# Performance work log

Hardware: AMD Instinct MI355X
Metric: run time of the kernel (lower is better)

The kernel has to match this reference:

```python
import jax, jax.numpy as jnp
import numpy as np

LN_EPS = 1e-5

def _layer_norm(x, g, b):
    mu = jnp.mean(x, axis=-1, keepdims=True)
    var = jnp.mean(jnp.square(x - mu), axis=-1, keepdims=True)
    return (x - mu) * jax.lax.rsqrt(var + LN_EPS) * g + b

def setup_inputs() -> dict:
    key = jax.random.key(0)
    ks = jax.random.split(key, 12)
    B, L, E, H, W = 4, 1024, 1024, 16, 128
    s = 0.02
    return {
        "x": jax.random.normal(ks[0], (B, L, E), dtype=jnp.float32),
        "in_proj_w": jax.random.normal(ks[1], (3 * E, E), dtype=jnp.float32) * s,
        "in_proj_b": jnp.zeros((3 * E,), dtype=jnp.float32),
        "out_proj_w": jax.random.normal(ks[2], (E, E), dtype=jnp.float32) * s,
        "out_proj_b": jnp.zeros((E,), dtype=jnp.float32),
        "ln1_g": jnp.ones((E,), dtype=jnp.float32),
        "ln1_b": jnp.zeros((E,), dtype=jnp.float32),
        "w1": jax.random.normal(ks[3], (4 * E, E), dtype=jnp.float32) * s,
        "b1": jnp.zeros((4 * E,), dtype=jnp.float32),
        "w2": jax.random.normal(ks[4], (E, 4 * E), dtype=jnp.float32) * s,
        "b2": jnp.zeros((E,), dtype=jnp.float32),
        "ln2_g": jnp.ones((E,), dtype=jnp.float32),
        "ln2_b": jnp.zeros((E,), dtype=jnp.float32),
        "n_head": 16,
        "window_size": 128,
    }

def reference(x, in_proj_w, in_proj_b, out_proj_w, out_proj_b,
              ln1_g, ln1_b, w1, b1, w2, b2, ln2_g, ln2_b,
              n_head, window_size):
    B, L, E = x.shape
    H = n_head
    D = E // H
    # qkv projection (torch Linear convention: y = x @ W.T + b)
    qkv = jnp.einsum('ble,fe->blf', x, in_proj_w) + in_proj_b  # [B,L,3E]
    q, k, v = jnp.split(qkv, 3, axis=-1)
    q = q.reshape(B, L, H, D).transpose(0, 2, 1, 3)  # [B,H,L,D]
    k = k.reshape(B, L, H, D).transpose(0, 2, 1, 3)
    v = v.reshape(B, L, H, D).transpose(0, 2, 1, 3)
    scores = jnp.einsum('bhld,bhmd->bhlm', q, k) / np.sqrt(D)  # [B,H,L,L]
    # banded window mask: allowed iff |i-j| <= window_size (same as the double loop)
    idx = jnp.arange(L)
    band = jnp.abs(idx[:, None] - idx[None, :]) <= window_size  # [L,L]
    scores = jnp.where(band[None, None], scores, -jnp.inf)
    attn = jax.nn.softmax(scores, axis=-1)  # [B,H,L,L]
    ctx = jnp.einsum('bhlm,bhmd->bhld', attn, v)  # [B,H,L,D]
    ctx = ctx.transpose(0, 2, 1, 3).reshape(B, L, E)
    attn_out = jnp.einsum('ble,fe->blf', ctx, out_proj_w) + out_proj_b
    attn_weights = jnp.mean(attn, axis=1)  # torch MHA averages heads -> [B,L,L]
    # residual + norm1 (dropout is identity in eval)
    h = _layer_norm(x + attn_out, ln1_g, ln1_b)
    # positionwise FFN
    ff = jnp.einsum('ble,fe->blf', h, w1) + b1
    ff = jax.nn.relu(ff)
    ff = jnp.einsum('blf,ef->ble', ff, w2) + b2
    out = _layer_norm(h + ff, ln2_g, ln2_b)
    return (out, attn_weights)
```

## Files before the change

kernel.cpp:

```cpp
#include <hip/hip_runtime.h>

#define BB 4
#define LL 1024
#define EE 1024
#define HH 16
#define DD 64

typedef __attribute__((ext_vector_type(8))) short short8;
typedef __attribute__((ext_vector_type(4))) float floatx4;

#define PSTR ((size_t)4096 * 1024)

__device__ __forceinline__ float bf2f(short s) {
    union { unsigned u; float f; } c;
    c.u = ((unsigned)(unsigned short)s) << 16;
    return c.f;
}
__device__ __forceinline__ short f2bf(float f) {
    union { float f; unsigned u; } c; c.f = f;
    unsigned r = c.u + 0x7fffu + ((c.u >> 16) & 1u);
    return (short)(r >> 16);
}

__device__ __forceinline__ void async_copy16(const void* g, void* l) {
    __builtin_amdgcn_global_load_lds(
        (const __attribute__((address_space(1))) unsigned int*)g,
        (__attribute__((address_space(3))) unsigned int*)l, 16, 0, 0);
}

__global__ __launch_bounds__(256) void cvt5(
    const float* __restrict__ x, const float* __restrict__ wqkv,
    const float* __restrict__ wo, const float* __restrict__ w1,
    const float* __restrict__ w2,
    short* __restrict__ xb, short* __restrict__ wqkvb, short* __restrict__ wob,
    short* __restrict__ w1b, short* __restrict__ w2b)
{
    int bi = blockIdx.x;
    const float* in; short* out; int base;
    if      (bi <  4096) { in = x;    out = xb;    base = 0;     }
    else if (bi <  7168) { in = wqkv; out = wqkvb; base = 4096;  }
    else if (bi <  8192) { in = wo;   out = wob;   base = 7168;  }
    else if (bi < 12288) { in = w1;   out = w1b;   base = 8192;  }
    else                 { in = w2;   out = w2b;   base = 12288; }
    int i = (bi - base) * 256 + threadIdx.x;
    float4 v = ((const float4*)in)[i];
    unsigned long long u =
          (unsigned long long)(unsigned short)f2bf(v.x)
        | ((unsigned long long)(unsigned short)f2bf(v.y) << 16)
        | ((unsigned long long)(unsigned short)f2bf(v.z) << 32)
        | ((unsigned long long)(unsigned short)f2bf(v.w) << 48);
    ((unsigned long long*)out)[i] = u;
}

template<bool RELU, bool SK>
__global__ __launch_bounds__(512, 2) void gemm256(
    const short* __restrict__ A, const short* __restrict__ Bw,
    const float* __restrict__ bias,
    short* __restrict__ Cb,
    int M, int N, int K, int Ksp)
{
    __shared__ short SH[67584];
    const int tid  = threadIdx.x;
    const int w    = tid >> 6, lane = tid & 63;
    const int fr   = lane & 15, quad = lane >> 4;
    const int wm   = w >> 2,  wn   = w & 3;

    const int gx   = gridDim.x;
    const int flat = blockIdx.y * gx + blockIdx.x;
    const int nwg  = gx * gridDim.y;
    const int q8   = nwg >> 3;
    const int swz  = (flat & 7) * q8 + (flat >> 3);
    const int m0   = (swz % gx) * 256;
    const int n0   = (swz / gx) * 256;

    const int kb = SK ? blockIdx.z * Ksp : 0;
    const int NT = (SK ? Ksp : K) >> 6;

    const int srow = w * 16 + (lane >> 3);
    const int gcol = ((lane & 7) ^ ((lane >> 3) & 7)) * 8;

    auto stage = [&](int s, int h) {
        if (s >= NT) return;
        short* dstb = SH + (s & 1) * 32768 + (h >> 1) * 16384 + (h & 1) * 8192 + w * 1024;
        const short* src = (h < 2)
            ? A  + (size_t)(m0 + h * 128 + srow) * K + kb + s * 64 + gcol
            : Bw + (size_t)(n0 + (h - 2) * 128 + srow) * K + kb + s * 64 + gcol;
        async_copy16(src, dstb);
        async_copy16(src + (size_t)8 * K, dstb + 512);
    };

    floatx4 acc[8][4];
#pragma unroll
    for (int i = 0; i < 8; ++i)
#pragma unroll
        for (int j = 0; j < 4; ++j) acc[i][j] = (floatx4){0.f, 0.f, 0.f, 0.f};

    stage(0, 0); stage(0, 1); stage(0, 2); stage(0, 3);
    asm volatile("s_waitcnt vmcnt(0)" ::: "memory");
    __builtin_amdgcn_s_barrier();

    const int posk0 = ((quad    ) ^ (fr & 7)) * 8;
    const int posk1 = ((4 + quad) ^ (fr & 7)) * 8;

    for (int t = 0; t < NT; ++t) {
        const short* sA = SH + (t & 1) * 32768 + wm * 8192;
        const short* sB = SH + (t & 1) * 32768 + 16384 + wn * 4096;

        short8 aL[4], aH[4], b0[4], b1[4], a2[4], a3[4];

#pragma unroll
        for (int i = 0; i < 4; ++i) aL[i] = *(const short8*)&sA[(i * 16 + fr) * 64 + posk0];
#pragma unroll
        for (int j = 0; j < 4; ++j) b0[j] = *(const short8*)&sB[(j * 16 + fr) * 64 + posk0];
        stage(t + 1, 0); stage(t + 1, 1);
        __builtin_amdgcn_s_barrier();
        asm volatile("s_waitcnt lgkmcnt(0)" ::: "memory");
        __builtin_amdgcn_sched_barrier(0);
        __builtin_amdgcn_s_setprio(1);
#pragma unroll
        for (int i = 0; i < 4; ++i)
#pragma unroll
            for (int j = 0; j < 4; ++j)
                acc[i][j] = __builtin_amdgcn_mfma_f32_16x16x32_bf16(aL[i], b0[j], acc[i][j], 0, 0, 0);
        __builtin_amdgcn_s_setprio(0);
        __builtin_amdgcn_sched_barrier(0);
        __builtin_amdgcn_s_barrier();

#pragma unroll
        for (int i = 0; i < 4; ++i) aH[i] = *(const short8*)&sA[((i + 4) * 16 + fr) * 64 + posk0];
        stage(t + 1, 2); stage(t + 1, 3);
        __builtin_amdgcn_s_barrier();
        asm volatile("s_waitcnt lgkmcnt(0)" ::: "memory");
        __builtin_amdgcn_sched_barrier(0);
        __builtin_amdgcn_s_setprio(1);
#pragma unroll
        for (int i = 0; i < 4; ++i)
#pragma unroll
            for (int j = 0; j < 4; ++j)
                acc[i + 4][j] = __builtin_amdgcn_mfma_f32_16x16x32_bf16(aH[i], b0[j], acc[i + 4][j], 0, 0, 0);
        __builtin_amdgcn_s_setprio(0);
        __builtin_amdgcn_sched_barrier(0);
        __builtin_amdgcn_s_barrier();

#pragma unroll
        for (int i = 0; i < 4; ++i) a2[i] = *(const short8*)&sA[(i * 16 + fr) * 64 + posk1];
#pragma unroll
        for (int j = 0; j < 4; ++j) b1[j] = *(const short8*)&sB[(j * 16 + fr) * 64 + posk1];
        __builtin_amdgcn_s_barrier();
        asm volatile("s_waitcnt lgkmcnt(0)" ::: "memory");
        __builtin_amdgcn_sched_barrier(0);
        __builtin_amdgcn_s_setprio(1);
#pragma unroll
        for (int i = 0; i < 4; ++i)
#pragma unroll
            for (int j = 0; j < 4; ++j)
                acc[i][j] = __builtin_amdgcn_mfma_f32_16x16x32_bf16(a2[i], b1[j], acc[i][j], 0, 0, 0);
        __builtin_amdgcn_s_setprio(0);
        __builtin_amdgcn_sched_barrier(0);
        __builtin_amdgcn_s_barrier();

#pragma unroll
        for (int i = 0; i < 4; ++i) a3[i] = *(const short8*)&sA[((i + 4) * 16 + fr) * 64 + posk1];
        asm volatile("s_waitcnt vmcnt(0)" ::: "memory");
        __builtin_amdgcn_s_barrier();
        asm volatile("s_waitcnt lgkmcnt(0)" ::: "memory");
        __builtin_amdgcn_sched_barrier(0);
        __builtin_amdgcn_s_setprio(1);
#pragma unroll
        for (int i = 0; i < 4; ++i)
#pragma unroll
            for (int j = 0; j < 4; ++j)
                acc[i + 4][j] = __builtin_amdgcn_mfma_f32_16x16x32_bf16(a3[i], b1[j], acc[i + 4][j], 0, 0, 0);
        __builtin_amdgcn_s_setprio(0);
        __builtin_amdgcn_sched_barrier(0);
        __builtin_amdgcn_s_barrier();
    }

    __syncthreads();

    const int cc = lane & 15, rb4 = quad * 4;
#pragma unroll
    for (int i = 0; i < 8; ++i) {
        int row = wm * 128 + i * 16 + rb4;
#pragma unroll
        for (int j = 0; j < 4; ++j) {
            int col = wn * 64 + j * 16 + cc;
            float bv = SK ? 0.0f : bias[n0 + col];
#pragma unroll
            for (int r = 0; r < 4; ++r) {
                float v = acc[i][j][r] + bv;
                if (RELU) v = fmaxf(v, 0.0f);
                SH[(row + r) * 264 + col] = f2bf(v);
            }
        }
    }
    __syncthreads();
    short* Co = Cb + (SK ? (size_t)blockIdx.z * PSTR : 0);
#pragma unroll
    for (int it = 0; it < 16; ++it) {
        int idx = it * 512 + tid;
        int row = idx >> 5, ch = idx & 31;
        short8 v = *(const short8*)&SH[row * 264 + ch * 8];
        *(short8*)&Co[(size_t)(m0 + row) * N + n0 + ch * 8] = v;
    }
}

__global__ __launch_bounds__(256) void vtrans(const short* __restrict__ qkv,
                                              short* __restrict__ vt)
{
    int id = blockIdx.x;
    int tb = id & 15, h = (id >> 4) & 15, b = id >> 8;
    __shared__ short T[64 * 72];
    const short* src = qkv + (size_t)(b * 1024 + tb * 64) * 3072 + 2048 + h * 64;
    int tok = threadIdx.x >> 2;
    int c8  = threadIdx.x & 3;
#pragma unroll
    for (int q = 0; q < 2; ++q) {
        int d0 = (c8 * 2 + q) * 8;
        short8 v = *(const short8*)&src[(size_t)tok * 3072 + d0];
#pragma unroll
        for (int e = 0; e < 8; ++e) T[(d0 + e) * 72 + tok] = v[e];
    }
    __syncthreads();
    short* dst = vt + (size_t)((b * 16 + h) * 64) * 1024 + tb * 64;
    int d = threadIdx.x >> 2, cq = threadIdx.x & 3;
#pragma unroll
    for (int q = 0; q < 2; ++q) {
        int t0 = (cq * 2 + q) * 8;
        *(short8*)&dst[(size_t)d * 1024 + t0] = *(const short8*)&T[d * 72 + t0];
    }
}

template<bool RELU, bool SK>
__global__ __launch_bounds__(256) void gemm_bt(
    const short* __restrict__ A, const short* __restrict__ Bw,
    const float* __restrict__ bias,
    short* __restrict__ Cb,
    int M, int N, int K, int Ksp)
{
    __shared__ union U {
        struct { short As[128 * 64]; short Bs[128 * 64]; } s;
        short Cs[128 * 136];
    } u;
    const int tid  = threadIdx.x;
    const int wave = tid >> 6, lane = tid & 63;
    const int m0 = blockIdx.x * 128, n0 = blockIdx.y * 128;
    const int wm = (wave & 1) * 64, wn = (wave >> 1) * 64;
    const int kbase = SK ? blockIdx.z * Ksp : 0;

    floatx4 acc[4][4];
#pragma unroll
    for (int i = 0; i < 4; ++i)
#pragma unroll
        for (int j = 0; j < 4; ++j) acc[i][j] = (floatx4){0.f, 0.f, 0.f, 0.f};

    const int srow = wave * 8 + (lane >> 3);
    const int scol = (((lane & 7) ^ ((lane >> 3) & 7))) * 8;
    const short* gA = A  + (size_t)(m0 + srow) * K + kbase + scol;
    const short* gB = Bw + (size_t)(n0 + srow) * K + kbase + scol;
    short* lA = u.s.As + wave * 512;
    short* lB = u.s.Bs + wave * 512;

    const int fr = lane & 15, quad = lane >> 4;
    const int kiters = (SK ? Ksp : K) >> 6;
    for (int kt = 0; kt < kiters; ++kt) {
#pragma unroll
        for (int s = 0; s < 4; ++s) {
            async_copy16(gA + (size_t)s * 32 * K, lA + s * 2048);
            async_copy16(gB + (size_t)s * 32 * K, lB + s * 2048);
        }
        gA += 64; gB += 64;
        __syncthreads();
#pragma unroll
        for (int ks = 0; ks < 2; ++ks) {
            short8 af[4], bf[4];
#pragma unroll
            for (int i = 0; i < 4; ++i) {
                int pos = ((ks * 4 + quad) ^ (fr & 7)) * 8;
                af[i] = *(const short8*)&u.s.As[(wm + i * 16 + fr) * 64 + pos];
                bf[i] = *(const short8*)&u.s.Bs[(wn + i * 16 + fr) * 64 + pos];
            }
#pragma unroll
            for (int i = 0; i < 4; ++i)
#pragma unroll
                for (int j = 0; j < 4; ++j)
                    acc[i][j] = __builtin_amdgcn_mfma_f32_16x16x32_bf16(af[i], bf[j], acc[i][j], 0, 0, 0);
        }
        __syncthreads();
    }

    const int cc = lane & 15;
    const int rb = (lane >> 4) * 4;
#pragma unroll
    for (int j = 0; j < 4; ++j) {
        int col = wn + j * 16 + cc;
        float bv = SK ? 0.0f : bias[n0 + col];
#pragma unroll
        for (int i = 0; i < 4; ++i) {
            int row = wm + i * 16 + rb;
#pragma unroll
            for (int r = 0; r < 4; ++r) {
                float v = acc[i][j][r] + bv;
                if (RELU) v = fmaxf(v, 0.0f);
                u.Cs[(row + r) * 136 + col] = f2bf(v);
            }
        }
    }
    __syncthreads();
    short* Co = Cb + (SK ? (size_t)blockIdx.z * PSTR : 0);
    const int trow = tid >> 4, tcol = (tid & 15) * 8;
#pragma unroll
    for (int p = 0; p < 8; ++p) {
        int row = p * 16 + trow;
        short8 vv = *(const short8*)&u.Cs[row * 136 + tcol];
        *(short8*)&Co[(size_t)(m0 + row) * N + n0 + tcol] = vv;
    }
}

__global__ __launch_bounds__(256) void ln_kernel(
    const float* __restrict__ xa, const short* __restrict__ parts, int nparts,
    const float* __restrict__ bias,
    const float* __restrict__ g, const float* __restrict__ beta,
    float* __restrict__ outf, short* __restrict__ outb)
{
    const int row = blockIdx.x;
    const int tid = threadIdx.x;
    float4 va = ((const float4*)(xa + (size_t)row * EE))[tid];
    float4 vb = ((const float4*)bias)[tid];
    float v0 = va.x + vb.x, v1 = va.y + vb.y, v2 = va.z + vb.z, v3 = va.w + vb.w;
#pragma unroll 4
    for (int p = 0; p < nparts; ++p) {
        unsigned long long u8 = ((const unsigned long long*)(parts + p * PSTR + (size_t)row * EE))[tid];
        v0 += bf2f((short)(u8 & 0xffff));
        v1 += bf2f((short)((u8 >> 16) & 0xffff));
        v2 += bf2f((short)((u8 >> 32) & 0xffff));
        v3 += bf2f((short)(u8 >> 48));
    }
    float s  = v0 + v1 + v2 + v3;
    float ss = v0 * v0 + v1 * v1 + v2 * v2 + v3 * v3;
#pragma unroll
    for (int o = 1; o < 64; o <<= 1) { s += __shfl_xor(s, o); ss += __shfl_xor(ss, o); }
    __shared__ float red[8];
    if ((tid & 63) == 0) { red[(tid >> 6) * 2] = s; red[(tid >> 6) * 2 + 1] = ss; }
    __syncthreads();
    s  = red[0] + red[2] + red[4] + red[6];
    ss = red[1] + red[3] + red[5] + red[7];
    float mean = s * (1.0f / EE);
    float var  = ss * (1.0f / EE) - mean * mean;
    float rstd = rsqrtf(var + 1e-5f);
    float4 vg = ((const float4*)g)[tid];
    float4 vt = ((const float4*)beta)[tid];
    float o0 = (v0 - mean) * rstd * vg.x + vt.x;
    float o1 = (v1 - mean) * rstd * vg.y + vt.y;
    float o2 = (v2 - mean) * rstd * vg.z + vt.z;
    float o3 = (v3 - mean) * rstd * vg.w + vt.w;
    if (outf) ((float4*)(outf + (size_t)row * EE))[tid] = make_float4(o0, o1, o2, o3);
    if (outb) {
        unsigned long long u =
              (unsigned long long)(unsigned short)f2bf(o0)
            | ((unsigned long long)(unsigned short)f2bf(o1) << 16)
            | ((unsigned long long)(unsigned short)f2bf(o2) << 32)
            | ((unsigned long long)(unsigned short)f2bf(o3) << 48);
        ((unsigned long long*)(outb + (size_t)row * EE))[tid] = u;
    }
}

__global__ __launch_bounds__(512, 8) void attn_mfma(
    const short* __restrict__ qkv,
    const short* __restrict__ vt,
    short* __restrict__ ctxp,
    short* __restrict__ pb)
{
    __shared__ short Pl[32 * 320];
    __shared__ float Red[4][2][32];
    const int tid = threadIdx.x, wave = tid >> 6, lane = tid & 63;
    const int quad = lane >> 4, mcol = lane & 15;
    const int id = blockIdx.x;
    const int i0 = (id >> 6) * 32, h = id & 15, b = (id >> 4) & 3;
    const int jb0 = i0 - 128;

    const short* qb = qkv + (size_t)(b * 1024) * 3072 + h * 64;
    const short* kb = qb + 1024;

    const int mt = wave >> 2, qtr = wave & 3;
    const short* qrow = qb + (size_t)(i0 + mt * 16 + mcol) * 3072 + quad * 8;
    short8 aq0 = *(const short8*)qrow;
    short8 aq1 = *(const short8*)(qrow + 32);

    floatx4 sacc[5];
#pragma unroll
    for (int c = 0; c < 5; ++c) sacc[c] = (floatx4){0.f, 0.f, 0.f, 0.f};
#pragma unroll
    for (int c = 0; c < 5; ++c) {
        int j = jb0 + (qtr * 5 + c) * 16 + mcol;
        j = min(max(j, 0), 1023);
        const short* kr = kb + (size_t)j * 3072 + quad * 8;
        short8 b0 = *(const short8*)kr;
        short8 b1 = *(const short8*)(kr + 32);
        sacc[c] = __builtin_amdgcn_mfma_f32_16x16x32_bf16(aq0, b0, sacc[c], 0, 0, 0);
        sacc[c] = __builtin_amdgcn_mfma_f32_16x16x32_bf16(aq1, b1, sacc[c], 0, 0, 0);
    }

    const int row0 = mt * 16 + quad * 4;
#pragma unroll
    for (int r = 0; r < 4; ++r) {
        int row = row0 + r;
        float m = -1e30f;
#pragma unroll
        for (int c = 0; c < 5; ++c) {
            int jo = (qtr * 5 + c) * 16 + mcol;
            bool val = (jo >= row) && (jo <= row + 256) && ((unsigned)(jb0 + jo) < 1024u);
            float s = val ? sacc[c][r] * 0.125f : -1e30f;
            sacc[c][r] = s;
            m = fmaxf(m, s);
        }
        m = fmaxf(m, __shfl_xor(m, 1));
        m = fmaxf(m, __shfl_xor(m, 2));
        m = fmaxf(m, __shfl_xor(m, 4));
        m = fmaxf(m, __shfl_xor(m, 8));
        if (mcol == 0) Red[qtr][0][row] = m;
    }
    __syncthreads();
#pragma unroll
    for (int r = 0; r < 4; ++r) {
        int row = row0 + r;
        float M = fmaxf(fmaxf(Red[0][0][row], Red[1][0][row]),
                        fmaxf(Red[2][0][row], Red[3][0][row]));
        float l = 0.f;
#pragma unroll
        for (int c = 0; c < 5; ++c) {
            float p = __expf(sacc[c][r] - M);
            sacc[c][r] = p;
            l += p;
        }
        l += __shfl_xor(l, 1);
        l += __shfl_xor(l, 2);
        l += __shfl_xor(l, 4);
        l += __shfl_xor(l, 8);
        if (mcol == 0) Red[qtr][1][row] = l;
    }
    __syncthreads();
#pragma unroll
    for (int r = 0; r < 4; ++r) {
        int row = row0 + r;
        float inv = 1.0f / (Red[0][1][row] + Red[1][1][row] +
                            Red[2][1][row] + Red[3][1][row]);
#pragma unroll
        for (int c = 0; c < 5; ++c) {
            int jo = (qtr * 5 + c) * 16 + mcol;
            Pl[row * 320 + (((jo >> 3) ^ (row & 7)) * 8) + (jo & 7)] = f2bf(sacc[c][r] * inv);
        }
    }
    __syncthreads();

    const int pmt = wave & 1, dt = wave >> 1;
    floatx4 cacc = (floatx4){0.f, 0.f, 0.f, 0.f};
    const short* vrow = vt + ((size_t)((b * 16 + h) * 64) + dt * 16 + mcol) * 1024;
    const int prow = (pmt * 16 + mcol) * 320;
#pragma unroll
    for (int jc = 0; jc < 10; ++jc) {
        short8 ap = *(const short8*)&Pl[prow + (((jc * 4 + quad) ^ (mcol & 7)) * 8)];
        int jg = jb0 + jc * 32 + quad * 8;
        if ((unsigned)jg >= 1024u) jg = 0;
        short8 bv = *(const short8*)(vrow + jg);
        cacc = __builtin_amdgcn_mfma_f32_16x16x32_bf16(ap, bv, cacc, 0, 0, 0);
    }

    short* pbb = pb + ((size_t)((b * 16 + h) * 1024) + i0) * 320;
    for (int t = tid; t < 1280; t += 512) {
        int row = t / 40, c = t - row * 40;
        short8 v = *(const short8*)&Pl[row * 320 + ((c ^ (row & 7)) * 8)];
        *(short8*)&pbb[(size_t)t * 8] = v;
    }
    __syncthreads();

    short* Ct = Pl;
    const int colc = dt * 16 + mcol;
#pragma unroll
    for (int r = 0; r < 4; ++r)
        Ct[(pmt * 16 + quad * 4 + r) * 72 + colc] = f2bf(cacc[r]);
    __syncthreads();
    short* cb = ctxp + (size_t)(b * 1024 + i0) * 1024 + h * 64;
    for (int t = tid; t < 256; t += 512) {
        int row = t >> 3, c = t & 7;
        short8 v = *(const short8*)&Ct[row * 72 + c * 8];
        *(short8*)&cb[(size_t)row * 1024 + c * 8] = v;
    }
}

__global__ __launch_bounds__(256) void pb_reduce(const short* __restrict__ pb,
                                                 float* __restrict__ aw)
{
    const int i = blockIdx.x & 1023, b = blockIdx.x >> 10;
    const int i0 = i & ~31;
    __shared__ short P[16 * 320];
    for (int t = threadIdx.x; t < 640; t += 256) {
        int hh = t / 40, c = t - hh * 40;
        ((short8*)P)[t] = *(const short8*)(pb +
            ((size_t)((b * 16 + hh) * 1024) + i) * 320 + c * 8);
    }
    __syncthreads();
    float* row = aw + ((size_t)(b * 1024) + i) * 1024;
    for (int j = threadIdx.x; j < 1024; j += 256) {
        int jo = j - i0 + 128;
        float s = 0.f;
        if ((unsigned)jo < 320u) {
#pragma unroll
            for (int hh = 0; hh < 16; ++hh)
                s += bf2f(P[hh * 320 + jo]);
            s *= (1.0f / 16.0f);
        }
        row[j] = s;
    }
}

extern "C" void kernel_launch(void* const* d_in, const int* in_sizes, int n_in,
                              void* d_out, int out_size, void* d_ws, size_t ws_size,
                              hipStream_t stream) {
    const float* x    = (const float*)d_in[0];
    const float* wqkv = (const float*)d_in[1];
    const float* bqkv = (const float*)d_in[2];
    const float* wo   = (const float*)d_in[3];
    const float* bo   = (const float*)d_in[4];
    const float* g1   = (const float*)d_in[5];
    const float* be1  = (const float*)d_in[6];
    const float* w1   = (const float*)d_in[7];
    const float* bb1  = (const float*)d_in[8];
    const float* w2   = (const float*)d_in[9];
    const float* bb2  = (const float*)d_in[10];
    const float* g2   = (const float*)d_in[11];
    const float* be2  = (const float*)d_in[12];

    char* ws = (char*)d_ws;
    size_t off = 0;
    auto take = [&](size_t bytes) {
        void* p = ws + off;
        off += (bytes + 255) & ~(size_t)255;
        return p;
    };
    short* xb     = (short*)take((size_t)4096 * 1024 * 2);
    short* wqkv_b = (short*)take((size_t)3072 * 1024 * 2);
    short* wo_b   = (short*)take((size_t)1024 * 1024 * 2);
    short* w1_b   = (short*)take((size_t)4096 * 1024 * 2);
    short* w2_b   = (short*)take((size_t)1024 * 4096 * 2);
    short* qkv_b  = (short*)take((size_t)4096 * 3072 * 2);
    short* ctx_b  = (short*)take((size_t)4096 * 1024 * 2);
    short* ff2_p  = qkv_b;
    short* attn_p = (short*)take((size_t)2 * 4096 * 1024 * 2);
    float* h_f    = (float*)take((size_t)4096 * 1024 * 4);
    short* vt_ws  = (short*)h_f;
    short* h_b    = (short*)take((size_t)4096 * 1024 * 2);
    short* pb_ws  = (short*)take((size_t)4 * 16 * 1024 * 320 * 2);
    short* ff_b   = pb_ws;

    float* out_f = (float*)d_out;
    float* attnW = (float*)d_out + (size_t)4 * 1024 * 1024;

    cvt5<<<16384, 256, 0, stream>>>(x, wqkv, wo, w1, w2, xb, wqkv_b, wo_b, w1_b, w2_b);

    gemm256<false, false><<<dim3(16, 12), 512, 0, stream>>>(
        xb, wqkv_b, bqkv, qkv_b, 4096, 3072, 1024, 1024);

    vtrans<<<1024, 256, 0, stream>>>(qkv_b, vt_ws);

    attn_mfma<<<2048, 512, 0, stream>>>(qkv_b, vt_ws, ctx_b, pb_ws);

    pb_reduce<<<4096, 256, 0, stream>>>(pb_ws, attnW);

    gemm_bt<false, true><<<dim3(32, 8, 2), 256, 0, stream>>>(
        ctx_b, wo_b, nullptr, attn_p, 4096, 1024, 1024, 512);

    ln_kernel<<<4096, 256, 0, stream>>>(x, attn_p, 2, bo, g1, be1, h_f, h_b);

    gemm256<true, false><<<dim3(16, 16), 512, 0, stream>>>(
        h_b, w1_b, bb1, ff_b, 4096, 4096, 1024, 1024);

    gemm256<false, true><<<dim3(16, 4, 4), 512, 0, stream>>>(
        ff_b, w2_b, nullptr, ff2_p, 4096, 1024, 4096, 1024);

    ln_kernel<<<4096, 256, 0, stream>>>(h_f, ff2_p, 4, bb2, g2, be2, out_f, nullptr);
}
```

Before: 342.6 us.

## Restructure GEMM pipeline barriers and enlarge attention query tile with LDS-staged K

The GEMM main loop now issues all four next-stage async copies at once and waits for global loads at the top of each iteration, removing several block barriers per K step. The attention kernel now handles 64 query rows per block instead of 32: it stages the 320-row K window into swizzled shared memory with async copies and reuses it across more query rows, and each wave computes two V output tiles. This halves the block count and cuts redundant global K reads, at the cost of more registers and LDS per block and fewer resident blocks (launch bounds lowered). The pb_reduce indexing changes to match the new 64-row tiling.

```diff
diff --git a/kernel.cpp b/kernel.cpp
--- a/kernel.cpp
+++ b/kernel.cpp
@@ -96,24 +96,39 @@
         for (int j = 0; j < 4; ++j) acc[i][j] = (floatx4){0.f, 0.f, 0.f, 0.f};
 
     stage(0, 0); stage(0, 1); stage(0, 2); stage(0, 3);
-    asm volatile("s_waitcnt vmcnt(0)" ::: "memory");
-    __builtin_amdgcn_s_barrier();
 
     const int posk0 = ((quad    ) ^ (fr & 7)) * 8;
     const int posk1 = ((4 + quad) ^ (fr & 7)) * 8;
 
     for (int t = 0; t < NT; ++t) {
+        asm volatile("s_waitcnt vmcnt(0)" ::: "memory");
+        __builtin_amdgcn_sched_barrier(0);
+        __builtin_amdgcn_s_barrier();
+
         const short* sA = SH + (t & 1) * 32768 + wm * 8192;
         const short* sB = SH + (t & 1) * 32768 + 16384 + wn * 4096;
 
-        short8 aL[4], aH[4], b0[4], b1[4], a2[4], a3[4];
+        short8 aL[4], aH[4], b0v[4], b1v[4], a2[4], a3[4];
 
 #pragma unroll
         for (int i = 0; i < 4; ++i) aL[i] = *(const short8*)&sA[(i * 16 + fr) * 64 + posk0];
 #pragma unroll
-        for (int j = 0; j < 4; ++j) b0[j] = *(const short8*)&sB[(j * 16 + fr) * 64 + posk0];
-        stage(t + 1, 0); stage(t + 1, 1);
+        for (int j = 0; j < 4; ++j) b0v[j] = *(const short8*)&sB[(j * 16 + fr) * 64 + posk0];
+        stage(t + 1, 0); stage(t + 1, 1); stage(t + 1, 2); stage(t + 1, 3);
+        asm volatile("s_waitcnt lgkmcnt(0)" ::: "memory");
+        __builtin_amdgcn_sched_barrier(0);
+        __builtin_amdgcn_s_setprio(1);
+#pragma unroll
+        for (int i = 0; i < 4; ++i)
+#pragma unroll
+            for (int j = 0; j < 4; ++j)
+                acc[i][j] = __builtin_amdgcn_mfma_f32_16x16x32_bf16(aL[i], b0v[j], acc[i][j], 0, 0, 0);
+        __builtin_amdgcn_s_setprio(0);
+        __builtin_amdgcn_sched_barrier(0);
         __builtin_amdgcn_s_barrier();
+
+#pragma unroll
+        for (int i = 0; i < 4; ++i) aH[i] = *(const short8*)&sA[((i + 4) * 16 + fr) * 64 + posk0];
         asm volatile("s_waitcnt lgkmcnt(0)" ::: "memory");
         __builtin_amdgcn_sched_barrier(0);
         __builtin_amdgcn_s_setprio(1);
@@ -121,15 +136,29 @@
         for (int i = 0; i < 4; ++i)
 #pragma unroll
             for (int j = 0; j < 4; ++j)
-                acc[i][j] = __builtin_amdgcn_mfma_f32_16x16x32_bf16(aL[i], b0[j], acc[i][j], 0, 0, 0);
+                acc[i + 4][j] = __builtin_amdgcn_mfma_f32_16x16x32_bf16(aH[i], b0v[j], acc[i + 4][j], 0, 0, 0);
         __builtin_amdgcn_s_setprio(0);
         __builtin_amdgcn_sched_barrier(0);
         __builtin_amdgcn_s_barrier();
 
 #pragma unroll
-        for (int i = 0; i < 4; ++i) aH[i] = *(const short8*)&sA[((i + 4) * 16 + fr) * 64 + posk0];
-        stage(t + 1, 2); stage(t + 1, 3);
+        for (int i = 0; i < 4; ++i) a2[i] = *(const short8*)&sA[(i * 16 + fr) * 64 + posk1];
+#pragma unroll
+        for (int j = 0; j < 4; ++j) b1v[j] = *(const short8*)&sB[(j * 16 + fr) * 64 + posk1];
+        asm volatile("s_waitcnt lgkmcnt(0)" ::: "memory");
+        __builtin_amdgcn_sched_barrier(0);
+        __builtin_amdgcn_s_setprio(1);
+#pragma unroll
+        for (int i = 0; i < 4; ++i)
+#pragma unroll
+            for (int j = 0; j < 4; ++j)
+                acc[i][j] = __builtin_amdgcn_mfma_f32_16x16x32_bf16(a2[i], b1v[j], acc[i][j], 0, 0, 0);
+        __builtin_amdgcn_s_setprio(0);
+        __builtin_amdgcn_sched_barrier(0);
         __builtin_amdgcn_s_barrier();
+
+#pragma unroll
+        for (int i = 0; i < 4; ++i) a3[i] = *(const short8*)&sA[((i + 4) * 16 + fr) * 64 + posk1];
         asm volatile("s_waitcnt lgkmcnt(0)" ::: "memory");
         __builtin_amdgcn_sched_barrier(0);
         __builtin_amdgcn_s_setprio(1);
@@ -137,43 +166,9 @@
         for (int i = 0; i < 4; ++i)
 #pragma unroll
             for (int j = 0; j < 4; ++j)
-                acc[i + 4][j] = __builtin_amdgcn_mfma_f32_16x16x32_bf16(aH[i], b0[j], acc[i + 4][j], 0, 0, 0);
+                acc[i + 4][j] = __builtin_amdgcn_mfma_f32_16x16x32_bf16(a3[i], b1v[j], acc[i + 4][j], 0, 0, 0);
         __builtin_amdgcn_s_setprio(0);
         __builtin_amdgcn_sched_barrier(0);
-        __builtin_amdgcn_s_barrier();
-
-#pragma unroll
-        for (int i = 0; i < 4; ++i) a2[i] = *(const short8*)&sA[(i * 16 + fr) * 64 + posk1];
-#pragma unroll
-        for (int j = 0; j < 4; ++j) b1[j] = *(const short8*)&sB[(j * 16 + fr) * 64 + posk1];
-        __builtin_amdgcn_s_barrier();
-        asm volatile("s_waitcnt lgkmcnt(0)" ::: "memory");
-        __builtin_amdgcn_sched_barrier(0);
-        __builtin_amdgcn_s_setprio(1);
-#pragma unroll
-        for (int i = 0; i < 4; ++i)
-#pragma unroll
-            for (int j = 0; j < 4; ++j)
-                acc[i][j] = __builtin_amdgcn_mfma_f32_16x16x32_bf16(a2[i], b1[j], acc[i][j], 0, 0, 0);
-        __builtin_amdgcn_s_setprio(0);
-        __builtin_amdgcn_sched_barrier(0);
-        __builtin_amdgcn_s_barrier();
-
-#pragma unroll
-        for (int i = 0; i < 4; ++i) a3[i] = *(const short8*)&sA[((i + 4) * 16 + fr) * 64 + posk1];
-        asm volatile("s_waitcnt vmcnt(0)" ::: "memory");
-        __builtin_amdgcn_s_barrier();
-        asm volatile("s_waitcnt lgkmcnt(0)" ::: "memory");
-        __builtin_amdgcn_sched_barrier(0);
-        __builtin_amdgcn_s_setprio(1);
-#pragma unroll
-        for (int i = 0; i < 4; ++i)
-#pragma unroll
-            for (int j = 0; j < 4; ++j)
-                acc[i + 4][j] = __builtin_amdgcn_mfma_f32_16x16x32_bf16(a3[i], b1[j], acc[i + 4][j], 0, 0, 0);
-        __builtin_amdgcn_s_setprio(0);
-        __builtin_amdgcn_sched_barrier(0);
-        __builtin_amdgcn_s_barrier();
     }
 
     __syncthreads();
@@ -365,38 +360,50 @@
     }
 }
 
-__global__ __launch_bounds__(512, 8) void attn_mfma(
+__global__ __launch_bounds__(512, 4) void attn_mfma(
     const short* __restrict__ qkv,
     const short* __restrict__ vt,
     short* __restrict__ ctxp,
     short* __restrict__ pb)
 {
-    __shared__ short Pl[32 * 320];
-    __shared__ float Red[4][2][32];
-    const int tid = threadIdx.x, wave = tid >> 6, lane = tid & 63;
+    __shared__ short Kl[64 * 320];
+    __shared__ float Red[2][2][64];
+    const int tid = threadIdx.x, w = tid >> 6, lane = tid & 63;
     const int quad = lane >> 4, mcol = lane & 15;
     const int id = blockIdx.x;
-    const int i0 = (id >> 6) * 32, h = id & 15, b = (id >> 4) & 3;
+    const int i0 = (id >> 6) * 64, h = id & 15, b = (id >> 4) & 3;
     const int jb0 = i0 - 128;
 
     const short* qb = qkv + (size_t)(b * 1024) * 3072 + h * 64;
     const short* kb = qb + 1024;
 
-    const int mt = wave >> 2, qtr = wave & 3;
+    {
+        short* dstb = Kl + w * 512;
+#pragma unroll
+        for (int it = 0; it < 5; ++it) {
+            int jo = it * 64 + w * 8 + (lane >> 3);
+            int j  = min(max(jb0 + jo, 0), 1023);
+            int g  = (lane & 7) ^ (jo & 7);
+            async_copy16(kb + (size_t)j * 3072 + g * 8, dstb + it * 4096);
+        }
+    }
+
+    const int mt = w >> 1, qtr = w & 1;
     const short* qrow = qb + (size_t)(i0 + mt * 16 + mcol) * 3072 + quad * 8;
     short8 aq0 = *(const short8*)qrow;
     short8 aq1 = *(const short8*)(qrow + 32);
 
-    floatx4 sacc[5];
-#pragma unroll
-    for (int c = 0; c < 5; ++c) sacc[c] = (floatx4){0.f, 0.f, 0.f, 0.f};
-#pragma unroll
-    for (int c = 0; c < 5; ++c) {
-        int j = jb0 + (qtr * 5 + c) * 16 + mcol;
-        j = min(max(j, 0), 1023);
-        const short* kr = kb + (size_t)j * 3072 + quad * 8;
-        short8 b0 = *(const short8*)kr;
-        short8 b1 = *(const short8*)(kr + 32);
+    __syncthreads();
+
+    floatx4 sacc[10];
+#pragma unroll
+    for (int c = 0; c < 10; ++c) sacc[c] = (floatx4){0.f, 0.f, 0.f, 0.f};
+#pragma unroll
+    for (int c = 0; c < 10; ++c) {
+        int jo = qtr * 160 + c * 16 + mcol;
+        const short* krow = Kl + jo * 64;
+        short8 b0 = *(const short8*)&krow[((quad    ) ^ (jo & 7)) * 8];
+        short8 b1 = *(const short8*)&krow[((4 + quad) ^ (jo & 7)) * 8];
         sacc[c] = __builtin_amdgcn_mfma_f32_16x16x32_bf16(aq0, b0, sacc[c], 0, 0, 0);
         sacc[c] = __builtin_amdgcn_mfma_f32_16x16x32_bf16(aq1, b1, sacc[c], 0, 0, 0);
     }
@@ -407,8 +414,8 @@
         int row = row0 + r;
         float m = -1e30f;
 #pragma unroll
-        for (int c = 0; c < 5; ++c) {
-            int jo = (qtr * 5 + c) * 16 + mcol;
+        for (int c = 0; c < 10; ++c) {
+            int jo = qtr * 160 + c * 16 + mcol;
             bool val = (jo >= row) && (jo <= row + 256) && ((unsigned)(jb0 + jo) < 1024u);
             float s = val ? sacc[c][r] * 0.125f : -1e30f;
             sacc[c][r] = s;
@@ -424,11 +431,10 @@
 #pragma unroll
     for (int r = 0; r < 4; ++r) {
         int row = row0 + r;
-        float M = fmaxf(fmaxf(Red[0][0][row], Red[1][0][row]),
-                        fmaxf(Red[2][0][row], Red[3][0][row]));
+        float M = fmaxf(Red[0][0][row], Red[1][0][row]);
         float l = 0.f;
 #pragma unroll
-        for (int c = 0; c < 5; ++c) {
+        for (int c = 0; c < 10; ++c) {
             float p = __expf(sacc[c][r] - M);
             sacc[c][r] = p;
             l += p;
@@ -440,49 +446,56 @@
         if (mcol == 0) Red[qtr][1][row] = l;
     }
     __syncthreads();
+    short* Pl = Kl;
 #pragma unroll
     for (int r = 0; r < 4; ++r) {
         int row = row0 + r;
-        float inv = 1.0f / (Red[0][1][row] + Red[1][1][row] +
-                            Red[2][1][row] + Red[3][1][row]);
-#pragma unroll
-        for (int c = 0; c < 5; ++c) {
-            int jo = (qtr * 5 + c) * 16 + mcol;
+        float inv = 1.0f / (Red[0][1][row] + Red[1][1][row]);
+#pragma unroll
+        for (int c = 0; c < 10; ++c) {
+            int jo = qtr * 160 + c * 16 + mcol;
             Pl[row * 320 + (((jo >> 3) ^ (row & 7)) * 8) + (jo & 7)] = f2bf(sacc[c][r] * inv);
         }
     }
     __syncthreads();
 
-    const int pmt = wave & 1, dt = wave >> 1;
-    floatx4 cacc = (floatx4){0.f, 0.f, 0.f, 0.f};
-    const short* vrow = vt + ((size_t)((b * 16 + h) * 64) + dt * 16 + mcol) * 1024;
+    const int pmt = w & 3, dth = w >> 2;
+    floatx4 cacc[2];
+    cacc[0] = (floatx4){0.f, 0.f, 0.f, 0.f};
+    cacc[1] = (floatx4){0.f, 0.f, 0.f, 0.f};
     const int prow = (pmt * 16 + mcol) * 320;
+    const short* vb0 = vt + ((size_t)((b * 16 + h) * 64 + dth * 32) + mcol) * 1024;
 #pragma unroll
     for (int jc = 0; jc < 10; ++jc) {
         short8 ap = *(const short8*)&Pl[prow + (((jc * 4 + quad) ^ (mcol & 7)) * 8)];
         int jg = jb0 + jc * 32 + quad * 8;
         if ((unsigned)jg >= 1024u) jg = 0;
-        short8 bv = *(const short8*)(vrow + jg);
-        cacc = __builtin_amdgcn_mfma_f32_16x16x32_bf16(ap, bv, cacc, 0, 0, 0);
+        short8 bv0 = *(const short8*)(vb0 + jg);
+        short8 bv1 = *(const short8*)(vb0 + (size_t)16 * 1024 + jg);
+        cacc[0] = __builtin_amdgcn_mfma_f32_16x16x32_bf16(ap, bv0, cacc[0], 0, 0, 0);
+        cacc[1] = __builtin_amdgcn_mfma_f32_16x16x32_bf16(ap, bv1, cacc[1], 0, 0, 0);
     }
 
     short* pbb = pb + ((size_t)((b * 16 + h) * 1024) + i0) * 320;
-    for (int t = tid; t < 1280; t += 512) {
+#pragma unroll
+    for (int s = 0; s < 5; ++s) {
+        int t = s * 512 + tid;
         int row = t / 40, c = t - row * 40;
         short8 v = *(const short8*)&Pl[row * 320 + ((c ^ (row & 7)) * 8)];
         *(short8*)&pbb[(size_t)t * 8] = v;
     }
     __syncthreads();
 
-    short* Ct = Pl;
-    const int colc = dt * 16 + mcol;
-#pragma unroll
-    for (int r = 0; r < 4; ++r)
-        Ct[(pmt * 16 + quad * 4 + r) * 72 + colc] = f2bf(cacc[r]);
+    short* Ct = Kl;
+#pragma unroll
+    for (int d2 = 0; d2 < 2; ++d2)
+#pragma unroll
+        for (int r = 0; r < 4; ++r)
+            Ct[(pmt * 16 + quad * 4 + r) * 72 + dth * 32 + d2 * 16 + mcol] = f2bf(cacc[d2][r]);
     __syncthreads();
     short* cb = ctxp + (size_t)(b * 1024 + i0) * 1024 + h * 64;
-    for (int t = tid; t < 256; t += 512) {
-        int row = t >> 3, c = t & 7;
+    {
+        int row = tid >> 3, c = tid & 7;
         short8 v = *(const short8*)&Ct[row * 72 + c * 8];
         *(short8*)&cb[(size_t)row * 1024 + c * 8] = v;
     }
@@ -492,7 +505,7 @@
                                                  float* __restrict__ aw)
 {
     const int i = blockIdx.x & 1023, b = blockIdx.x >> 10;
-    const int i0 = i & ~31;
+    const int i0 = i & ~63;
     __shared__ short P[16 * 320];
     for (int t = threadIdx.x; t < 640; t += 256) {
         int hh = t / 40, c = t - hh * 40;
@@ -563,7 +576,7 @@
 
     vtrans<<<1024, 256, 0, stream>>>(qkv_b, vt_ws);
 
-    attn_mfma<<<2048, 512, 0, stream>>>(qkv_b, vt_ws, ctx_b, pb_ws);
+    attn_mfma<<<1024, 512, 0, stream>>>(qkv_b, vt_ws, ctx_b, pb_ws);
 
     pb_reduce<<<4096, 256, 0, stream>>>(pb_ws, attnW);
 
```

Measured after the change: 325.5 us. 5.0% less time.
